# Kernel optimization log

Hardware: AMD Instinct MI355X
Metric: run time of the kernel (lower is better)

The kernel has to match this reference:

```python
import jax, jax.numpy as jnp
import numpy as np

N_NODES = 200000
N_EDGES = 800000
N_GRAPHS = 8192
NFEAT = 74
FP = 1024
H = 4   # num heads
F = 50  # feats per head
BN_EPS = 1e-5
ATTN_SLOPE = 0.2     # GATConv leaky-relu alpha
ACT_SLOPE = 0.01     # nn.LeakyReLU() default after layer 1
CAPS_COEF = 1.0 / np.sqrt(128.0)  # 1/sqrt(D), D=128


def squash2(x, axis=-1):
    sq = (x ** 2).sum(axis=axis, keepdims=True)
    return (1.0 - 1.0 / jnp.exp(jnp.sqrt(sq))) * x / jnp.sqrt(sq + 1e-8)


def gat_layer(x, src, dst, W, attn_l, attn_r, bias, res_W):
    # x: [N, in] -> feat: [N, H, F]
    feat = (x @ W).reshape(N_NODES, H, F)
    el = (feat * attn_l).sum(-1)            # [N, H]
    er = (feat * attn_r).sum(-1)            # [N, H]
    e = jax.nn.leaky_relu(el[src] + er[dst], ATTN_SLOPE)  # [E, H]
    # edge softmax over incoming edges of each dst node
    m = jax.ops.segment_max(e, dst, num_segments=N_NODES)
    a = jnp.exp(e - m[dst])
    denom = jax.ops.segment_sum(a, dst, num_segments=N_NODES)
    alpha = a / denom[dst]                  # [E, H]
    out = jax.ops.segment_sum(alpha[:, :, None] * feat[src], dst,
                              num_segments=N_NODES)  # [N, H, F]
    if res_W is None:
        res = x.reshape(N_NODES, H, F)      # identity residual (in == H*F)
    else:
        res = (x @ res_W).reshape(N_NODES, H, F)
    return out + res + bias.reshape(1, H, F)


def setup_inputs():
    key = jax.random.key(0)
    ks = jax.random.split(key, 24)
    h = jax.random.normal(ks[0], (N_NODES, NFEAT), jnp.float32)
    fps = (jax.random.uniform(ks[1], (N_GRAPHS, FP)) < 0.1).astype(jnp.float32)
    src = jax.random.randint(ks[2], (N_EDGES,), 0, N_NODES)
    dst = jax.random.randint(ks[3], (N_EDGES,), 0, N_NODES)
    # sorted graph assignment, every graph non-empty
    graph_id = (jnp.arange(N_NODES) * N_GRAPHS) // N_NODES
    s = 0.05
    p = lambda i, shp: s * jax.random.normal(ks[i], shp, jnp.float32)
    return dict(
        h=h, fps=fps, src=src, dst=dst, graph_id=graph_id,
        W1=p(4, (NFEAT, H * F)), al1=p(5, (H, F)), ar1=p(6, (H, F)),
        b1=p(7, (H * F,)), resW1=p(8, (NFEAT, H * F)),
        W2=p(9, (H * F, H * F)), al2=p(10, (H, F)), ar2=p(11, (H, F)),
        b2=p(12, (H * F,)),
        lw1=p(13, (F + FP, 128)), lb1=p(14, (128,)),
        bn_g=jnp.ones((128,), jnp.float32), bn_b=jnp.zeros((128,), jnp.float32),
        bn_rm=jnp.zeros((128,), jnp.float32), bn_rv=jnp.ones((128,), jnp.float32),
        lw2=p(15, (128, 128)), lb2=p(16, (128,)),
        capsW=0.01 * jax.random.normal(ks[17], (2, 16, 2, 8), jnp.float32),
        capsB=0.01 * jax.random.normal(ks[18], (2, 1, 16), jnp.float32),
    )


def reference(h, fps, src, dst, graph_id, W1, al1, ar1, b1, resW1,
              W2, al2, ar2, b2, lw1, lb1, bn_g, bn_b, bn_rm, bn_rv,
              lw2, lb2, capsW, capsB):
    # ---- GAT layer 1: flatten heads + LeakyReLU ----
    x = gat_layer(h, src, dst, W1, al1, ar1, b1, resW1).reshape(N_NODES, H * F)
    x = jax.nn.leaky_relu(x, ACT_SLOPE)
    # ---- GAT layer 2: mean over heads, no activation ----
    x = gat_layer(x, src, dst, W2, al2, ar2, b2, None).mean(axis=1)  # [N, F]
    # ---- MaxPooling per graph ----
    g = jax.ops.segment_max(x, graph_id, num_segments=N_GRAPHS)  # [G, F]
    # ---- MLP head (eval mode: dropout off, BN uses running stats) ----
    z = jnp.concatenate([g, fps], axis=-1)
    z = jax.nn.relu(z @ lw1 + lb1)
    z = (z - bn_rm) / jnp.sqrt(bn_rv + BN_EPS) * bn_g + bn_b
    z = jax.nn.relu(z @ lw2 + lb2)                                # [G, 128]
    # ---- PrimaryCaps2: view (G, 16, 8), squash ----
    u = squash2(z.reshape(N_GRAPHS, 16, 8))
    # ---- DigitCaps2 ----
    # u_hat[b,n,c,d] = sum_e W[n,c,d,e] * u[b,c,e]
    u_hat = jnp.einsum('ncde,bce->bncd', capsW, u)                # [G,2,16,2]
    a = CAPS_COEF * jnp.einsum('bncd,bnkd->bnck', u_hat, u_hat)   # [G,2,16,16]
    c = jax.nn.softmax(a.sum(axis=-2, keepdims=True), axis=1)     # [G,2,1,16]
    s = jnp.matmul(c + capsB, u_hat).squeeze(-2)                  # [G,2,2]
    v = squash2(s)
    return jnp.sqrt((v ** 2).sum(-1) + 1e-8)                      # [G,2]
```

## Files before the change

### kernel.cpp

```cpp
#include <hip/hip_runtime.h>
#include <hip/hip_bf16.h>

#define NN 200000
#define NE 800000
#define NG 8192
#define KIN 74
#define FPD 1024
#define HF 200
#define FF 50

typedef float f4 __attribute__((ext_vector_type(4)));
typedef __hip_bfloat16 bf16;
typedef __attribute__((ext_vector_type(8))) short sh8;
typedef __attribute__((ext_vector_type(4))) float f32x4;

__device__ __forceinline__ unsigned short f2bf(float f) {
    unsigned u = __float_as_uint(f);
    u += 0x7fffu + ((u >> 16) & 1u);
    return (unsigned short)(u >> 16);
}
__device__ __forceinline__ float bflo(unsigned u) { return __uint_as_float(u << 16); }
__device__ __forceinline__ float bfhi(unsigned u) { return __uint_as_float(u & 0xffff0000u); }
__device__ __forceinline__ unsigned pack2(float a, float b) {
    return (unsigned)f2bf(a) | ((unsigned)f2bf(b) << 16);
}

__global__ __launch_bounds__(256)
void k_prep_a(const float* __restrict__ h, unsigned* __restrict__ hp)
{
    int idx = blockIdx.x * 256 + threadIdx.x;
    if (idx >= NN * 48) return;
    int row = idx / 48, c2 = idx - row * 48;
    int k = 2 * c2;
    float v0 = (k     < KIN) ? h[(size_t)row * KIN + k]     : 0.f;
    float v1 = (k + 1 < KIN) ? h[(size_t)row * KIN + k + 1] : 0.f;
    hp[idx] = pack2(v0, v1);
}

__global__ __launch_bounds__(256)
void k_prep_bt(const float* __restrict__ W, unsigned short* __restrict__ Bt,
               int K, int N, int kPad, int nColPad, int colOff)
{
    int idx = blockIdx.x * 256 + threadIdx.x;
    if (idx >= nColPad * kPad) return;
    int col = idx / kPad, k = idx - col * kPad;
    float v = (col < N && k < K) ? W[(size_t)k * N + col] : 0.f;
    Bt[(size_t)(colOff + col) * kPad + k] = f2bf(v);
}

__global__ __launch_bounds__(256)
void k_prep_fps(const float* __restrict__ fps, unsigned* __restrict__ zb)
{
    int idx = blockIdx.x * 256 + threadIdx.x;
    if (idx >= NG * 519) return;
    int g = idx / 519, dw = 25 + (idx - g * 519);
    int c0 = 2 * dw - 50;
    float v0 = (c0     < FPD) ? fps[(size_t)g * FPD + c0]     : 0.f;
    float v1 = (c0 + 1 < FPD) ? fps[(size_t)g * FPD + c0 + 1] : 0.f;
    zb[(size_t)g * 544 + dw] = pack2(v0, v1);
}

template<int KCH>
__global__ __launch_bounds__(256)
void gemm_mfma(const unsigned short* __restrict__ A, int lda,
               const unsigned short* __restrict__ Bt,
               const float* __restrict__ bias2,
               bf16* __restrict__ C1, bf16* __restrict__ C2)
{
    const int t = threadIdx.x;
    const int lane = t & 63, w = t >> 6;
    const int l15 = lane & 15, l4 = lane >> 4;
    const int kPad = KCH * 32;
    const int mat = blockIdx.y;
    const int row0 = blockIdx.x * 64 + w * 16;
    const unsigned short* ap = A + (size_t)(row0 + l15) * lda + l4 * 8;
    const unsigned short* bp = Bt + (size_t)mat * 208 * kPad
                                  + (size_t)l15 * kPad + l4 * 8;
    f32x4 acc[13] = {};

    #pragma unroll 2
    for (int kc = 0; kc < KCH; ++kc) {
        sh8 a = *(const sh8*)(ap + kc * 32);
        #pragma unroll
        for (int ct = 0; ct < 13; ++ct) {
            sh8 b = *(const sh8*)(bp + (size_t)ct * 16 * kPad + kc * 32);
            acc[ct] = __builtin_amdgcn_mfma_f32_16x16x32_bf16(a, b, acc[ct], 0, 0, 0);
        }
    }

    bf16* C = mat ? C2 : C1;
    const bool hasb = (mat == 1) && (bias2 != nullptr);
    #pragma unroll
    for (int ct = 0; ct < 13; ++ct) {
        int col = ct * 16 + l15;
        if (col < 200) {
            float bv = hasb ? bias2[col] : 0.f;
            #pragma unroll
            for (int j = 0; j < 4; ++j) {
                int row = row0 + l4 * 4 + j;
                C[(size_t)row * 200 + col] = __float2bfloat16(acc[ct][j] + bv);
            }
        }
    }
}

__global__ __launch_bounds__(256)
void gemm_mlp1(const unsigned short* __restrict__ A,
               const unsigned short* __restrict__ Bt,
               float* __restrict__ Cpart)
{
    const int t = threadIdx.x;
    const int lane = t & 63, w = t >> 6;
    const int l15 = lane & 15, l4 = lane >> 4;
    const int row0 = blockIdx.x * 64 + w * 16;
    const int c0   = blockIdx.y * 64;
    const int kz   = blockIdx.z;
    const unsigned short* ap = A + (size_t)(row0 + l15) * 1088 + kz * 544 + l4 * 8;
    const unsigned short* bp = Bt + (size_t)(c0 + l15) * 1088 + kz * 544 + l4 * 8;
    f32x4 acc[4] = {};

    #pragma unroll 2
    for (int kc = 0; kc < 17; ++kc) {
        sh8 a = *(const sh8*)(ap + kc * 32);
        #pragma unroll
        for (int ct = 0; ct < 4; ++ct) {
            sh8 b = *(const sh8*)(bp + (size_t)ct * 16 * 1088 + kc * 32);
            acc[ct] = __builtin_amdgcn_mfma_f32_16x16x32_bf16(a, b, acc[ct], 0, 0, 0);
        }
    }

    float* Cp = Cpart + (size_t)kz * NG * 128;
    #pragma unroll
    for (int ct = 0; ct < 4; ++ct) {
        int col = c0 + ct * 16 + l15;
        #pragma unroll
        for (int j = 0; j < 4; ++j) {
            int row = row0 + l4 * 4 + j;
            Cp[(size_t)row * 128 + col] = acc[ct][j];
        }
    }
}

__global__ __launch_bounds__(256)
void k_mlp_post(const float* __restrict__ Cpart, const float* __restrict__ lb1,
                const float* __restrict__ bng, const float* __restrict__ bnb,
                const float* __restrict__ bnrm, const float* __restrict__ bnrv,
                bf16* __restrict__ z1b)
{
    int i = blockIdx.x * 256 + threadIdx.x;
    if (i >= NG * 128) return;
    int c = i & 127;
    float v = Cpart[i] + Cpart[(size_t)NG * 128 + i] + lb1[c];
    v = fmaxf(v, 0.f);
    v = (v - bnrm[c]) * rsqrtf(bnrv[c] + 1e-5f) * bng[c] + bnb[c];
    z1b[i] = __float2bfloat16(v);
}

__global__ __launch_bounds__(256)
void gemm_mlp2(const unsigned short* __restrict__ A,
               const unsigned short* __restrict__ Bt,
               const float* __restrict__ lb2,
               float* __restrict__ z2)
{
    const int t = threadIdx.x;
    const int lane = t & 63, w = t >> 6;
    const int l15 = lane & 15, l4 = lane >> 4;
    const int row0 = blockIdx.x * 64 + w * 16;
    const int c0   = blockIdx.y * 64;
    const unsigned short* ap = A + (size_t)(row0 + l15) * 128 + l4 * 8;
    const unsigned short* bp = Bt + (size_t)(c0 + l15) * 128 + l4 * 8;
    f32x4 acc[4] = {};

    #pragma unroll
    for (int kc = 0; kc < 4; ++kc) {
        sh8 a = *(const sh8*)(ap + kc * 32);
        #pragma unroll
        for (int ct = 0; ct < 4; ++ct) {
            sh8 b = *(const sh8*)(bp + (size_t)ct * 16 * 128 + kc * 32);
            acc[ct] = __builtin_amdgcn_mfma_f32_16x16x32_bf16(a, b, acc[ct], 0, 0, 0);
        }
    }

    #pragma unroll
    for (int ct = 0; ct < 4; ++ct) {
        int col = c0 + ct * 16 + l15;
        float bv = lb2[col];
        #pragma unroll
        for (int j = 0; j < 4; ++j) {
            int row = row0 + l4 * 4 + j;
            z2[(size_t)row * 128 + col] = fmaxf(acc[ct][j] + bv, 0.f);
        }
    }
}

__global__ __launch_bounds__(256)
void k_el_er(const bf16* __restrict__ feat,
             const float* __restrict__ al, const float* __restrict__ ar,
             float* __restrict__ el, float* __restrict__ er)
{
    int t = blockIdx.x * 256 + threadIdx.x;
    if (t >= NN * 4) return;
    int n = t >> 2, h = t & 3;
    const unsigned* fr = (const unsigned*)(feat + (size_t)n*HF) + h*25;
    const float* alp = al + h*FF;
    const float* arp = ar + h*FF;
    float sl = 0.f, sr = 0.f;
    #pragma unroll
    for (int i = 0; i < 25; ++i) {
        unsigned u = fr[i];
        float v0 = bflo(u), v1 = bfhi(u);
        sl += v0*alp[2*i] + v1*alp[2*i+1];
        sr += v0*arp[2*i] + v1*arp[2*i+1];
    }
    el[t] = sl; er[t] = sr;
}

__global__ __launch_bounds__(256)
void k_count(const int* __restrict__ dst, int* __restrict__ cnt)
{
    int e = blockIdx.x * 256 + threadIdx.x;
    if (e < NE) atomicAdd(&cnt[dst[e]], 1);
}

__global__ __launch_bounds__(256)
void k_scan_a(const int* __restrict__ cnt, int* __restrict__ offs, int* __restrict__ bsum)
{
    __shared__ int tmp[256];
    int t = threadIdx.x, i = blockIdx.x * 256 + t;
    int v = (i < NN) ? cnt[i] : 0;
    tmp[t] = v; __syncthreads();
    #pragma unroll
    for (int d = 1; d < 256; d <<= 1) {
        int add = (t >= d) ? tmp[t - d] : 0; __syncthreads();
        tmp[t] += add; __syncthreads();
    }
    if (i < NN) offs[i + 1] = tmp[t];
    if (t == 255) bsum[blockIdx.x] = tmp[255];
}

__global__ __launch_bounds__(1024)
void k_scan_b(int* __restrict__ bsum, int nb)
{
    __shared__ int tmp[1024];
    int t = threadIdx.x;
    tmp[t] = (t < nb) ? bsum[t] : 0; __syncthreads();
    #pragma unroll
    for (int d = 1; d < 1024; d <<= 1) {
        int add = (t >= d) ? tmp[t - d] : 0; __syncthreads();
        tmp[t] += add; __syncthreads();
    }
    if (t < nb) bsum[t] = (t == 0) ? 0 : tmp[t - 1];
}

__global__ __launch_bounds__(256)
void k_scan_c(const int* __restrict__ bsum, int* __restrict__ offs)
{
    int i = blockIdx.x * 256 + threadIdx.x;
    if (i < NN) offs[i + 1] += bsum[blockIdx.x];
    if (i == 0) offs[0] = 0;
}

__global__ __launch_bounds__(256)
void k_fill(const int* __restrict__ src, const int* __restrict__ dst,
            const int* __restrict__ offs,
            int* __restrict__ cnt, int* __restrict__ csr_s)
{
    int e = blockIdx.x * 256 + threadIdx.x;
    if (e >= NE) return;
    int d = dst[e];
    int p = offs[d] + atomicAdd(&cnt[d], 1);
    csr_s[p] = src[e];
}

template<int LAYER>
__global__ __launch_bounds__(256)
void k_gather(const int* __restrict__ offs, const int* __restrict__ csr_s,
              const f4* __restrict__ el4, const f4* __restrict__ er4,
              const bf16* __restrict__ feat, const bf16* __restrict__ resx,
              const float* __restrict__ b2,
              bf16* __restrict__ x1out, bf16* __restrict__ x2out)
{
    __shared__ float sb[4][204];
    const int wv   = threadIdx.x >> 6;
    const int lane = threadIdx.x & 63;
    const int wid  = blockIdx.x * 4 + wv;
    const int beg = offs[wid], end = offs[wid + 1];
    const int hl  = (lane >= 25) ? 1 : 0;
    const bool act = lane < 50;

    const f4 erv = er4[wid];
    const float er_lo = hl ? erv.y : erv.x;
    const float er_hi = hl ? erv.w : erv.z;

    float s_lo = 0.f, s_hi = 0.f;
    float a0 = 0.f, a1 = 0.f, a2 = 0.f, a3 = 0.f;

#define EDGE(ev, lo, hi) {                                                  \
        float xl = (hl ? (ev).y : (ev).x) + er_lo;                          \
        xl = xl >= 0.f ? xl : 0.2f * xl;                                    \
        float xh = (hl ? (ev).w : (ev).z) + er_hi;                          \
        xh = xh >= 0.f ? xh : 0.2f * xh;                                    \
        float wl = __builtin_expf(xl), wh = __builtin_expf(xh);             \
        s_lo += wl; s_hi += wh;                                             \
        a0 += wl * bflo(lo); a1 += wl * bfhi(lo);                           \
        a2 += wh * bflo(hi); a3 += wh * bfhi(hi); }

    int i = beg;
    for (; i + 4 <= end; i += 4) {
        const int sn0 = csr_s[i], sn1 = csr_s[i+1], sn2 = csr_s[i+2], sn3 = csr_s[i+3];
        const f4 ev0 = el4[sn0], ev1 = el4[sn1], ev2 = el4[sn2], ev3 = el4[sn3];
        unsigned lo0=0, lo1=0, lo2=0, lo3=0, hi0=0, hi1=0, hi2=0, hi3=0;
        if (act) {
            const unsigned* f0 = (const unsigned*)(feat + (size_t)sn0 * HF);
            const unsigned* f1 = (const unsigned*)(feat + (size_t)sn1 * HF);
            const unsigned* f2 = (const unsigned*)(feat + (size_t)sn2 * HF);
            const unsigned* f3 = (const unsigned*)(feat + (size_t)sn3 * HF);
            lo0 = f0[lane]; hi0 = f0[lane + 50];
            lo1 = f1[lane]; hi1 = f1[lane + 50];
            lo2 = f2[lane]; hi2 = f2[lane + 50];
            lo3 = f3[lane]; hi3 = f3[lane + 50];
        }
        EDGE(ev0, lo0, hi0) EDGE(ev1, lo1, hi1) EDGE(ev2, lo2, hi2) EDGE(ev3, lo3, hi3)
    }
    for (; i < end; ++i) {
        const int sn = csr_s[i];
        const f4 ev = el4[sn];
        unsigned lo = 0, hi = 0;
        if (act) {
            const unsigned* fr = (const unsigned*)(feat + (size_t)sn * HF);
            lo = fr[lane]; hi = fr[lane + 50];
        }
        EDGE(ev, lo, hi)
    }
#undef EDGE

    const float inv_lo = s_lo > 0.f ? 1.f / s_lo : 0.f;
    const float inv_hi = s_hi > 0.f ? 1.f / s_hi : 0.f;
    a0 *= inv_lo; a1 *= inv_lo; a2 *= inv_hi; a3 *= inv_hi;

    if (LAYER == 1) {
        if (act) {
            const unsigned* rr = (const unsigned*)(resx + (size_t)wid * HF);
            unsigned rlo = rr[lane], rhi = rr[lane + 50];
            float t0 = a0 + bflo(rlo), t1 = a1 + bfhi(rlo);
            float t2 = a2 + bflo(rhi), t3 = a3 + bfhi(rhi);
            t0 = t0 >= 0.f ? t0 : 0.01f * t0;
            t1 = t1 >= 0.f ? t1 : 0.01f * t1;
            t2 = t2 >= 0.f ? t2 : 0.01f * t2;
            t3 = t3 >= 0.f ? t3 : 0.01f * t3;
            unsigned* xo = (unsigned*)(x1out + (size_t)wid * HF);
            xo[lane]      = pack2(t0, t1);
            xo[lane + 50] = pack2(t2, t3);
        }
    } else {
        if (act) {
            const unsigned* rr = (const unsigned*)(resx + (size_t)wid * HF);
            unsigned rlo = rr[lane], rhi = rr[lane + 50];
            int j = 2 * lane;
            sb[wv][j]       = a0 + bflo(rlo) + b2[j];
            sb[wv][j + 1]   = a1 + bfhi(rlo) + b2[j + 1];
            sb[wv][j + 100] = a2 + bflo(rhi) + b2[j + 100];
            sb[wv][j + 101] = a3 + bfhi(rhi) + b2[j + 101];
        }
        __syncthreads();
        if (lane < 25) {
            int j = 2 * lane;
            float v0 = 0.25f * (sb[wv][j]   + sb[wv][j + 50] + sb[wv][j + 100] + sb[wv][j + 150]);
            float v1 = 0.25f * (sb[wv][j+1] + sb[wv][j + 51] + sb[wv][j + 101] + sb[wv][j + 151]);
            unsigned* xo = (unsigned*)(x2out + (size_t)wid * FF);
            xo[lane] = pack2(v0, v1);
        }
    }
}

__global__ __launch_bounds__(64)
void k_graph_max(const bf16* __restrict__ x2, bf16* __restrict__ zb)
{
    int g = blockIdx.x;
    int f = threadIdx.x;
    if (f >= FF) return;
    long start = ((long)g     * NN + NG - 1) / NG;
    long end   = ((long)(g+1) * NN + NG - 1) / NG;
    float mv = -3.4e38f;
    for (long n = start; n < end; ++n) mv = fmaxf(mv, __bfloat162float(x2[n*FF + f]));
    zb[(size_t)g*1088 + f] = __float2bfloat16(mv);
}

__global__ __launch_bounds__(256)
void k_caps(const float* __restrict__ z2, const float* __restrict__ capsW,
            const float* __restrict__ capsB, float* __restrict__ out)
{
    int g = blockIdx.x * 256 + threadIdx.x;
    if (g >= NG) return;
    const float* z = z2 + (size_t)g*128;
    float uh[2][16][2];
    #pragma unroll
    for (int c = 0; c < 16; ++c) {
        float x[8]; float sq = 0.f;
        #pragma unroll
        for (int e = 0; e < 8; ++e) { x[e] = z[c*8 + e]; sq += x[e]*x[e]; }
        float sn  = sqrtf(sq);
        float fct = (1.f - __builtin_expf(-sn)) / sqrtf(sq + 1e-8f);
        #pragma unroll
        for (int e = 0; e < 8; ++e) x[e] *= fct;
        #pragma unroll
        for (int n = 0; n < 2; ++n)
            #pragma unroll
            for (int d = 0; d < 2; ++d) {
                float s2 = 0.f;
                #pragma unroll
                for (int e = 0; e < 8; ++e) s2 += capsW[((n*16 + c)*2 + d)*8 + e] * x[e];
                uh[n][c][d] = s2;
            }
    }
    float asum[2][16];
    #pragma unroll
    for (int n = 0; n < 2; ++n) {
        float t0 = 0.f, t1 = 0.f;
        #pragma unroll
        for (int c = 0; c < 16; ++c) { t0 += uh[n][c][0]; t1 += uh[n][c][1]; }
        #pragma unroll
        for (int k = 0; k < 16; ++k)
            asum[n][k] = 0.08838834764831845f * (t0*uh[n][k][0] + t1*uh[n][k][1]);
    }
    float s[2][2] = {};
    #pragma unroll
    for (int k = 0; k < 16; ++k) {
        float m  = fmaxf(asum[0][k], asum[1][k]);
        float e0 = __builtin_expf(asum[0][k] - m);
        float e1 = __builtin_expf(asum[1][k] - m);
        float inv = 1.f / (e0 + e1);
        float c0 = e0*inv + capsB[k];
        float c1 = e1*inv + capsB[16 + k];
        s[0][0] += c0*uh[0][k][0]; s[0][1] += c0*uh[0][k][1];
        s[1][0] += c1*uh[1][k][0]; s[1][1] += c1*uh[1][k][1];
    }
    #pragma unroll
    for (int n = 0; n < 2; ++n) {
        float sq  = s[n][0]*s[n][0] + s[n][1]*s[n][1];
        float sn  = sqrtf(sq);
        float fct = (1.f - __builtin_expf(-sn)) / sqrtf(sq + 1e-8f);
        float v0 = fct*s[n][0], v1 = fct*s[n][1];
        out[g*2 + n] = sqrtf(v0*v0 + v1*v1 + 1e-8f);
    }
}

extern "C" void kernel_launch(void* const* d_in, const int* in_sizes, int n_in,
                              void* d_out, int out_size, void* d_ws, size_t ws_size,
                              hipStream_t stream)
{
    const float* h     = (const float*)d_in[0];
    const float* fps   = (const float*)d_in[1];
    const int*   src   = (const int*)d_in[2];
    const int*   dst   = (const int*)d_in[3];
    const float* W1    = (const float*)d_in[5];
    const float* al1   = (const float*)d_in[6];
    const float* ar1   = (const float*)d_in[7];
    const float* b1    = (const float*)d_in[8];
    const float* resW1 = (const float*)d_in[9];
    const float* W2    = (const float*)d_in[10];
    const float* al2   = (const float*)d_in[11];
    const float* ar2   = (const float*)d_in[12];
    const float* b2    = (const float*)d_in[13];
    const float* lw1   = (const float*)d_in[14];
    const float* lb1   = (const float*)d_in[15];
    const float* bn_g  = (const float*)d_in[16];
    const float* bn_b  = (const float*)d_in[17];
    const float* bn_rm = (const float*)d_in[18];
    const float* bn_rv = (const float*)d_in[19];
    const float* lw2   = (const float*)d_in[20];
    const float* lb2   = (const float*)d_in[21];
    const float* capsW = (const float*)d_in[22];
    const float* capsB = (const float*)d_in[23];
    float* out = (float*)d_out;

    const int NB1 = (NN + 255) / 256;

    char* w = (char*)d_ws;
    auto alloc = [&](size_t nbytes) { char* p = w; w += (nbytes + 255) & ~(size_t)255; return p; };
    bf16* featb = (bf16*)alloc((size_t)NN*HF*2);
    bf16* x1b   = (bf16*)alloc((size_t)NN*HF*2);
    bf16* x2b   = (bf16*)alloc((size_t)NN*FF*2);
    unsigned* hpad = (unsigned*)alloc((size_t)NN*48*4);
    float* el   = (float*)alloc((size_t)NN*4*4);
    float* er   = (float*)alloc((size_t)NN*4*4);
    int*  offs  = (int*)alloc((size_t)(NN+1)*4);
    int*  cnt   = (int*)alloc((size_t)NN*4);
    int*  bsum  = (int*)alloc((size_t)NB1*4);
    int*  csr_s = (int*)alloc((size_t)NE*4);
    unsigned short* bt1  = (unsigned short*)alloc((size_t)416*96*2);
    unsigned short* bt2  = (unsigned short*)alloc((size_t)208*224*2);
    unsigned short* btm1 = (unsigned short*)alloc((size_t)128*1088*2);
    unsigned short* btm2 = (unsigned short*)alloc((size_t)128*128*2);

    unsigned* zb    = hpad;
    float*    z1p   = (float*)(hpad + (size_t)NG*544);
    bf16*     z1b   = (bf16*)((char*)z1p + (size_t)2*NG*128*4);
    float*    z2    = (float*)((char*)z1b + (size_t)NG*128*2);

    if ((size_t)(w - (char*)d_ws) > ws_size) return;

    const dim3 B256(256);

    hipLaunchKernelGGL(k_prep_a, dim3((NN*48+255)/256), B256, 0, stream, h, hpad);
    hipLaunchKernelGGL(k_prep_bt, dim3((208*96+255)/256),   B256, 0, stream, W1,    bt1,  KIN,  200,   96, 208, 0);
    hipLaunchKernelGGL(k_prep_bt, dim3((208*96+255)/256),   B256, 0, stream, resW1, bt1,  KIN,  200,   96, 208, 208);
    hipLaunchKernelGGL(k_prep_bt, dim3((208*224+255)/256),  B256, 0, stream, W2,    bt2,  HF,   200,  224, 208, 0);
    hipLaunchKernelGGL(k_prep_bt, dim3((128*1088+255)/256), B256, 0, stream, lw1,   btm1, 1074, 128, 1088, 128, 0);
    hipLaunchKernelGGL(k_prep_bt, dim3((128*128+255)/256),  B256, 0, stream, lw2,   btm2, 128,  128,  128, 128, 0);

    hipMemsetAsync(cnt, 0, (size_t)NN*4, stream);
    hipLaunchKernelGGL(k_count,  dim3(3125), B256, 0, stream, dst, cnt);
    hipLaunchKernelGGL(k_scan_a, dim3(NB1),  B256, 0, stream, cnt, offs, bsum);
    hipLaunchKernelGGL(k_scan_b, dim3(1), dim3(1024), 0, stream, bsum, NB1);
    hipLaunchKernelGGL(k_scan_c, dim3(NB1),  B256, 0, stream, bsum, offs);
    hipMemsetAsync(cnt, 0, (size_t)NN*4, stream);
    hipLaunchKernelGGL(k_fill,   dim3(3125), B256, 0, stream, src, dst, offs, cnt, csr_s);

    hipLaunchKernelGGL((gemm_mfma<3>), dim3(3125, 2), B256, 0, stream,
        (const unsigned short*)hpad, 96, bt1, b1, featb, x1b);
    hipLaunchKernelGGL(k_el_er, dim3(3125), B256, 0, stream, featb, al1, ar1, el, er);
    hipLaunchKernelGGL((k_gather<1>), dim3(50000), B256, 0, stream,
        offs, csr_s, (const f4*)el, (const f4*)er, featb, x1b, nullptr, x1b, nullptr);

    hipLaunchKernelGGL((gemm_mfma<7>), dim3(3125, 1), B256, 0, stream,
        (const unsigned short*)x1b, 200, bt2, nullptr, featb, nullptr);
    hipLaunchKernelGGL(k_el_er, dim3(3125), B256, 0, stream, featb, al2, ar2, el, er);
    hipLaunchKernelGGL((k_gather<2>), dim3(50000), B256, 0, stream,
        offs, csr_s, (const f4*)el, (const f4*)er, featb, x1b, b2, nullptr, x2b);

    hipLaunchKernelGGL(k_graph_max, dim3(NG), dim3(64), 0, stream, x2b, (bf16*)zb);
    hipLaunchKernelGGL(k_prep_fps, dim3((NG*519+255)/256), B256, 0, stream, fps, zb);
    hipLaunchKernelGGL(gemm_mlp1, dim3(128, 2, 2), B256, 0, stream,
        (const unsigned short*)zb, btm1, z1p);
    hipLaunchKernelGGL(k_mlp_post, dim3((NG*128+255)/256), B256, 0, stream,
        z1p, lb1, bn_g, bn_b, bn_rm, bn_rv, z1b);
    hipLaunchKernelGGL(gemm_mlp2, dim3(128, 2), B256, 0, stream,
        (const unsigned short*)z1b, btm2, lb2, z2);
    hipLaunchKernelGGL(k_caps, dim3(32), B256, 0, stream, z2, capsW, capsB, out);
}
```

Baseline: 828.6 us.

## Stage GEMM weight tiles in LDS and split column tiles across launches

The node-feature GEMMs now copy their transposed weight slice into shared memory once per block and read MFMA B operands from LDS instead of global memory. Blocks grow to 512 threads covering 128 rows, and the 13 column tiles are split across two launches (7 and 6 tiles) to keep accumulator registers and the LDS footprint small. The aim is to cut repeated global and L1 traffic for weights and to raise occupancy. In exchange, each A row is now read twice, once per column-split launch, and the last block reads A rows past the node count; only the stores are guarded.

```diff
diff --git a/kernel.cpp b/kernel.cpp
--- a/kernel.cpp
+++ b/kernel.cpp
@@ -60,30 +60,48 @@
     zb[(size_t)g * 544 + dw] = pack2(v0, v1);
 }
 
-template<int KCH>
-__global__ __launch_bounds__(256)
+template<int KCH, int NCT, int COLOFF>
+__global__ __launch_bounds__(512)
 void gemm_mfma(const unsigned short* __restrict__ A, int lda,
                const unsigned short* __restrict__ Bt,
                const float* __restrict__ bias2,
                bf16* __restrict__ C1, bf16* __restrict__ C2)
 {
+    constexpr int kPad   = KCH * 32;
+    constexpr int pitchW = kPad / 2 + 4;
+    __shared__ unsigned Bs[NCT * 16 * pitchW];
     const int t = threadIdx.x;
     const int lane = t & 63, w = t >> 6;
     const int l15 = lane & 15, l4 = lane >> 4;
-    const int kPad = KCH * 32;
     const int mat = blockIdx.y;
-    const int row0 = blockIdx.x * 64 + w * 16;
+    const int row0 = blockIdx.x * 128 + w * 16;
+
+    {
+        const uint4* g4 = (const uint4*)(Bt + ((size_t)mat * 208 + COLOFF) * kPad);
+        constexpr int perCol = kPad / 8;
+        constexpr int tot = NCT * 16 * perCol;
+        #pragma unroll
+        for (int idx = 0; idx < (tot + 511) / 512; ++idx) {
+            int i = idx * 512 + t;
+            if (i < tot) {
+                int c = i / perCol, d = i - c * perCol;
+                uint4 v = g4[(size_t)c * perCol + d];
+                *(uint4*)&Bs[c * pitchW + 4 * d] = v;
+            }
+        }
+    }
+    __syncthreads();
+
     const unsigned short* ap = A + (size_t)(row0 + l15) * lda + l4 * 8;
-    const unsigned short* bp = Bt + (size_t)mat * 208 * kPad
-                                  + (size_t)l15 * kPad + l4 * 8;
-    f32x4 acc[13] = {};
-
-    #pragma unroll 2
+    const unsigned* bsBase = &Bs[l15 * pitchW + l4 * 4];
+    f32x4 acc[NCT] = {};
+
+    #pragma unroll
     for (int kc = 0; kc < KCH; ++kc) {
         sh8 a = *(const sh8*)(ap + kc * 32);
         #pragma unroll
-        for (int ct = 0; ct < 13; ++ct) {
-            sh8 b = *(const sh8*)(bp + (size_t)ct * 16 * kPad + kc * 32);
+        for (int ct = 0; ct < NCT; ++ct) {
+            sh8 b = *(const sh8*)(bsBase + ct * 16 * pitchW + kc * 16);
             acc[ct] = __builtin_amdgcn_mfma_f32_16x16x32_bf16(a, b, acc[ct], 0, 0, 0);
         }
     }
@@ -91,14 +109,15 @@
     bf16* C = mat ? C2 : C1;
     const bool hasb = (mat == 1) && (bias2 != nullptr);
     #pragma unroll
-    for (int ct = 0; ct < 13; ++ct) {
-        int col = ct * 16 + l15;
+    for (int ct = 0; ct < NCT; ++ct) {
+        int col = COLOFF + ct * 16 + l15;
         if (col < 200) {
             float bv = hasb ? bias2[col] : 0.f;
             #pragma unroll
             for (int j = 0; j < 4; ++j) {
                 int row = row0 + l4 * 4 + j;
-                C[(size_t)row * 200 + col] = __float2bfloat16(acc[ct][j] + bv);
+                if (row < NN)
+                    C[(size_t)row * 200 + col] = __float2bfloat16(acc[ct][j] + bv);
             }
         }
     }
@@ -501,6 +520,7 @@
     if ((size_t)(w - (char*)d_ws) > ws_size) return;
 
     const dim3 B256(256);
+    const dim3 B512(512);
 
     hipLaunchKernelGGL(k_prep_a, dim3((NN*48+255)/256), B256, 0, stream, h, hpad);
     hipLaunchKernelGGL(k_prep_bt, dim3((208*96+255)/256),   B256, 0, stream, W1,    bt1,  KIN,  200,   96, 208, 0);
@@ -517,13 +537,17 @@
     hipMemsetAsync(cnt, 0, (size_t)NN*4, stream);
     hipLaunchKernelGGL(k_fill,   dim3(3125), B256, 0, stream, src, dst, offs, cnt, csr_s);
 
-    hipLaunchKernelGGL((gemm_mfma<3>), dim3(3125, 2), B256, 0, stream,
+    hipLaunchKernelGGL((gemm_mfma<3,7,0>),   dim3(1563, 2), B512, 0, stream,
+        (const unsigned short*)hpad, 96, bt1, b1, featb, x1b);
+    hipLaunchKernelGGL((gemm_mfma<3,6,112>), dim3(1563, 2), B512, 0, stream,
         (const unsigned short*)hpad, 96, bt1, b1, featb, x1b);
     hipLaunchKernelGGL(k_el_er, dim3(3125), B256, 0, stream, featb, al1, ar1, el, er);
     hipLaunchKernelGGL((k_gather<1>), dim3(50000), B256, 0, stream,
         offs, csr_s, (const f4*)el, (const f4*)er, featb, x1b, nullptr, x1b, nullptr);
 
-    hipLaunchKernelGGL((gemm_mfma<7>), dim3(3125, 1), B256, 0, stream,
+    hipLaunchKernelGGL((gemm_mfma<7,7,0>),   dim3(1563, 1), B512, 0, stream,
+        (const unsigned short*)x1b, 200, bt2, nullptr, featb, nullptr);
+    hipLaunchKernelGGL((gemm_mfma<7,6,112>), dim3(1563, 1), B512, 0, stream,
         (const unsigned short*)x1b, 200, bt2, nullptr, featb, nullptr);
     hipLaunchKernelGGL(k_el_er, dim3(3125), B256, 0, stream, featb, al2, ar2, el, er);
     hipLaunchKernelGGL((k_gather<2>), dim3(50000), B256, 0, stream,
```

Measured after the change: 779.3 us. -5.9%, faster.
